# Optimization experiments

Measured on AMD Instinct MI355X. Metric: run time of the kernel, lower is better.

Reference implementation:

```python
import jax, jax.numpy as jnp
import numpy as np

B, NI, NA, D = 16, 2048, 2048, 256

def setup_inputs() -> dict:
    key = jax.random.key(0)
    k1, k2, k3 = jax.random.split(key, 3)
    input_seq = jax.random.normal(k1, (B, NI, D), dtype=jnp.float32)
    attendee_seq = jax.random.normal(k2, (B, NA, D), dtype=jnp.float32)
    # glorot-ish scale for bilinear weight
    W = jax.random.normal(k3, (D, D), dtype=jnp.float32) * (1.0 / np.sqrt(D))
    return {"input_seq": input_seq, "attendee_seq": attendee_seq, "W": W}

def reference(input_seq, attendee_seq, W):
    # bilinear scores: (x_i W) . a_j   -> [B, NI, NA]
    xW = jnp.einsum('bid,de->bie', input_seq, W)
    scores = jnp.einsum('bie,bje->bij', xW, attendee_seq)
    A = jax.nn.softmax(scores, axis=2)                 # softmax over attendee axis
    # weighted context: sum_j A[b,i,j] * v[b,j,:] -> [B, NI, D]
    attended = jnp.einsum('bij,bjd->bid', A, attendee_seq)
    return attended
```

## Files before the change

### kernel.cpp

```cpp
#include <hip/hip_runtime.h>
#include <hip/hip_bf16.h>

#define BB 16
#define NI 2048
#define NA 2048
#define DD 256
#define KVB 32
#define NT (NA / KVB)

typedef _Float16 half8 __attribute__((ext_vector_type(8)));
typedef __attribute__((ext_vector_type(16))) float f32x16;
typedef __attribute__((ext_vector_type(4))) float f32x4;
typedef __attribute__((ext_vector_type(4))) unsigned int uint4v;

typedef const unsigned int CGU __attribute__((address_space(1)));
typedef unsigned int LU __attribute__((address_space(3)));

static __device__ __forceinline__ unsigned short f2h(float f) {
  union { _Float16 h; unsigned short u; } x; x.h = (_Float16)f; return x.u;
}
static __device__ __forceinline__ float h2f(unsigned short u) {
  union { _Float16 h; unsigned short u; } x; x.u = u; return (float)x.h;
}
static __device__ __forceinline__ unsigned int pk2(float a, float b) {
  return __builtin_bit_cast(unsigned int, __builtin_amdgcn_cvt_pkrtz(a, b));
}
static __device__ __forceinline__ float ex2(float x) {
  return __builtin_amdgcn_exp2f(x);
}
static __device__ __forceinline__ void gload16(const unsigned short* g, unsigned short* l) {
  __builtin_amdgcn_global_load_lds((CGU*)g, (LU*)l, 16, 0, 0);
}

__global__ void prep_kernel(const float* __restrict__ a,
                            unsigned short* __restrict__ kfrag,
                            unsigned short* __restrict__ vfrag,
                            const float* __restrict__ w,
                            unsigned short* __restrict__ wbfh,
                            unsigned short* __restrict__ wbfl) {
  __shared__ float t[64][65];
  int bx = blockIdx.x;
  int tid = threadIdx.x;
  int rr = tid >> 4, c4 = tid & 15;

  if (bx >= 2048) {
    int r = bx - 2048;
    int dt = r >> 2, et4 = r & 3;
    int d0 = dt * 64, e0 = et4 * 64;
    int cc = c4 * 4;
#pragma unroll
    for (int k = 0; k < 4; ++k) {
      int row = rr + k * 16;
      float4 v = *(const float4*)(w + (size_t)(d0 + row) * DD + e0 + cc);
      t[row][cc + 0] = v.x; t[row][cc + 1] = v.y; t[row][cc + 2] = v.z; t[row][cc + 3] = v.w;
    }
    __syncthreads();
    int d = d0 + cc;
    int c = d >> 5;
    int quad = (d >> 3) & 3;
#pragma unroll
    for (int k = 0; k < 4; ++k) {
      int e_local = rr + k * 16;
      int eg = e0 + e_local;
      ushort4 h, l;
      float v0 = t[cc + 0][e_local]; h.x = f2h(v0); l.x = f2h(v0 - h2f(h.x));
      float v1 = t[cc + 1][e_local]; h.y = f2h(v1); l.y = f2h(v1 - h2f(h.y));
      float v2 = t[cc + 2][e_local]; h.z = f2h(v2); l.z = f2h(v2 - h2f(h.z));
      float v3 = t[cc + 3][e_local]; h.w = f2h(v3); l.w = f2h(v3 - h2f(h.w));
      int et = eg >> 4, l16e = eg & 15;
      size_t off = ((size_t)(et * 8 + c) * 64 + quad * 16 + l16e) * 8 + (c4 & 1) * 4;
      *(ushort4*)(wbfh + off) = h;
      *(ushort4*)(wbfl + off) = l;
    }
    return;
  }

  int b = bx >> 7;
  int r = bx & 127;
  int jt_t = r >> 2, dt_t = r & 3;
  int j0 = jt_t * 64, d0 = dt_t * 64;
#pragma unroll
  for (int k = 0; k < 4; ++k) {
    int row = rr + k * 16;
    int j = j0 + row;
    int d = d0 + c4 * 4;
    float4 v = *(const float4*)(a + ((size_t)b * NA + j) * DD + d);
    ushort4 hh;
    hh.x = f2h(v.x); hh.y = f2h(v.y); hh.z = f2h(v.z); hh.w = f2h(v.w);
    int kt = j >> 5;
    int ks = d >> 4;
    int lk = (j & 31) + 32 * ((d >> 3) & 1);
    *(ushort4*)(kfrag + (((size_t)b * NT + kt) * 16 + ks) * 512 + lk * 8 + (c4 & 1) * 4) = hh;
    t[row][c4 * 4 + 0] = v.x; t[row][c4 * 4 + 1] = v.y;
    t[row][c4 * 4 + 2] = v.z; t[row][c4 * 4 + 3] = v.w;
  }
  __syncthreads();
#pragma unroll
  for (int k = 0; k < 4; ++k) {
    int dl = rr + k * 16;
    int d = d0 + dl;
    int j = j0 + c4 * 4;
    ushort4 o;
    o.x = f2h(t[c4 * 4 + 0][dl]); o.y = f2h(t[c4 * 4 + 1][dl]);
    o.z = f2h(t[c4 * 4 + 2][dl]); o.w = f2h(t[c4 * 4 + 3][dl]);
    int kt = j >> 5;
    int hi = c4 & 1;
    int m = (c4 >> 2) & 1;
    int ebase = ((c4 >> 1) & 1) * 4;
    int hh_ = d >> 7, dtl = (d >> 5) & 3;
    int lv = (d & 31) + 32 * hi;
    *(ushort4*)(vfrag + ((((((size_t)b * NT + kt) * 2 + hh_) * 4 + dtl) * 2 + m) * 512) + lv * 8 + ebase) = o;
  }
}

__global__ __launch_bounds__(256, 8) void qgemm_kernel(
    const float* __restrict__ x, const unsigned short* __restrict__ wbfh,
    const unsigned short* __restrict__ wbfl, unsigned short* __restrict__ qfrag) {
  const int tid = threadIdx.x;
  const int lane = tid & 63;
  const int wv = tid >> 6;
  const int quad = lane >> 4;
  const int l16 = lane & 15;
  const int m0 = blockIdx.x * 64;

  half8 xf[8];
  {
    const float* xr = x + (size_t)(m0 + wv * 16 + l16) * DD;
#pragma unroll
    for (int c = 0; c < 8; ++c) {
      float4 a = *(const float4*)(xr + c * 32 + quad * 8);
      float4 b = *(const float4*)(xr + c * 32 + quad * 8 + 4);
      half8 v;
      v[0] = (_Float16)a.x; v[1] = (_Float16)a.y; v[2] = (_Float16)a.z; v[3] = (_Float16)a.w;
      v[4] = (_Float16)b.x; v[5] = (_Float16)b.y; v[6] = (_Float16)b.z; v[7] = (_Float16)b.w;
      xf[c] = v;
    }
  }

  const int sub = l16 & 7;
  const int khalf = (l16 >> 3) & 1;
#pragma unroll 1
  for (int et = 0; et < 16; ++et) {
    f32x4 acc; acc[0] = acc[1] = acc[2] = acc[3] = 0.f;
#pragma unroll
    for (int c = 0; c < 8; ++c) {
      half8 wh = *(const half8*)(wbfh + ((size_t)(et * 8 + c) * 64 + lane) * 8);
      half8 wl = *(const half8*)(wbfl + ((size_t)(et * 8 + c) * 64 + lane) * 8);
      acc = __builtin_amdgcn_mfma_f32_16x16x32_f16(xf[c], wh, acc, 0, 0, 0);
      acc = __builtin_amdgcn_mfma_f32_16x16x32_f16(xf[c], wl, acc, 0, 0, 0);
    }
#pragma unroll
    for (int rg = 0; rg < 4; ++rg) {
      int qrow = m0 + wv * 16 + 4 * quad + rg;
      int qt = qrow >> 5, l31q = qrow & 31;
      qfrag[((size_t)(qt * 16 + et)) * 512 + (l31q + 32 * khalf) * 8 + sub] =
          f2h(acc[rg] * 1.44269504f);
    }
  }
}

__global__ __launch_bounds__(256, 2) void attn_kernel(
    const unsigned short* __restrict__ kfrag, const unsigned short* __restrict__ vfrag,
    const unsigned short* __restrict__ qfrag, float* __restrict__ out) {
  __shared__ unsigned short kls[2][KVB * DD];

  const int tid = threadIdx.x;
  const int lane = tid & 63;
  const int wv = tid >> 6;
  const int pr = wv >> 1;
  const int h = wv & 1;
  const int l31 = lane & 31;
  const int hi = lane >> 5;

  int bx = blockIdx.x;
  int lbx = (bx & 7) * 64 + (bx >> 3);
  const int b = lbx >> 5;
  const int qbase = (lbx & 31) * 64 + pr * 32;

  const unsigned short* kfb = kfrag + (size_t)b * NT * 8192;

  half8 qh[16];
  {
    const unsigned short* qr = qfrag + ((size_t)((b * NI + qbase) >> 5) * 16) * 512 + lane * 8;
#pragma unroll
    for (int ks = 0; ks < 16; ++ks)
      qh[ks] = *(const half8*)(qr + ks * 512);
  }

  f32x16 acc[4];
#pragma unroll
  for (int dt = 0; dt < 4; ++dt)
#pragma unroll
    for (int i = 0; i < 16; ++i) acc[dt][i] = 0.f;
  float m0r = -INFINITY;
  float l0 = 0.f;

  const unsigned short* vp = vfrag + (((size_t)b * NT * 2 + h) * 4) * 1024 + lane * 8;
  const unsigned short* sp = kfb + 8192 + (wv * 512 + lane * 8);

#pragma unroll
  for (int i = 0; i < 4; ++i) {
    int off = (i * 4 + wv) * 512;
    gload16(kfb + off + lane * 8, &kls[0][off]);
  }
  __syncthreads();

#pragma unroll 1
  for (int kt = 0; kt < NT; ++kt) {
    half8 vb[8];
#pragma unroll
    for (int i = 0; i < 8; ++i)
      vb[i] = *(const half8*)(vp + i * 512);

    if (kt + 1 < NT) {
      unsigned short* d = &kls[(kt + 1) & 1][wv * 512];
      gload16(sp + 0 * 2048, d + 0 * 2048);
      gload16(sp + 1 * 2048, d + 1 * 2048);
      gload16(sp + 2 * 2048, d + 2 * 2048);
      gload16(sp + 3 * 2048, d + 3 * 2048);
    }

    const unsigned short* kb = &kls[kt & 1][0];
    f32x16 sA, sB;
#pragma unroll
    for (int i = 0; i < 16; ++i) { sA[i] = 0.f; sB[i] = 0.f; }
    __builtin_amdgcn_s_setprio(1);
#pragma unroll
    for (int ks = 0; ks < 8; ++ks) {
      half8 ka = *(const half8*)(kb + ks * 512 + lane * 8);
      sA = __builtin_amdgcn_mfma_f32_32x32x16_f16(ka, qh[ks], sA, 0, 0, 0);
    }
#pragma unroll
    for (int ks = 8; ks < 16; ++ks) {
      half8 ka = *(const half8*)(kb + ks * 512 + lane * 8);
      sB = __builtin_amdgcn_mfma_f32_32x32x16_f16(ka, qh[ks], sB, 0, 0, 0);
    }
    __builtin_amdgcn_s_setprio(0);
    float p[16];
#pragma unroll
    for (int i = 0; i < 16; ++i) p[i] = sA[i] + sB[i];

    float mt = p[0];
#pragma unroll
    for (int i = 1; i < 16; ++i) mt = fmaxf(mt, p[i]);
    mt = fmaxf(mt, __shfl_xor(mt, 32));
    if (__any(mt > m0r + 11.5416f)) {
      float mn = fmaxf(m0r, mt);
      float sc = ex2(m0r - mn);
      l0 *= sc;
#pragma unroll
      for (int dt = 0; dt < 4; ++dt)
#pragma unroll
        for (int i = 0; i < 16; ++i) acc[dt][i] *= sc;
      m0r = mn;
    }

#pragma unroll
    for (int i = 0; i < 16; ++i) p[i] = ex2(p[i] - m0r);
    l0 += (((p[0] + p[1]) + (p[2] + p[3])) + ((p[4] + p[5]) + (p[6] + p[7]))) +
          (((p[8] + p[9]) + (p[10] + p[11])) + ((p[12] + p[13]) + (p[14] + p[15])));

    half8 pa0, pa1;
    {
      uint4v u0 = { pk2(p[0], p[1]), pk2(p[2], p[3]), pk2(p[4], p[5]), pk2(p[6], p[7]) };
      uint4v u1 = { pk2(p[8], p[9]), pk2(p[10], p[11]), pk2(p[12], p[13]), pk2(p[14], p[15]) };
      pa0 = __builtin_bit_cast(half8, u0);
      pa1 = __builtin_bit_cast(half8, u1);
    }

    __builtin_amdgcn_s_setprio(1);
#pragma unroll
    for (int dt = 0; dt < 4; ++dt) {
      acc[dt] = __builtin_amdgcn_mfma_f32_32x32x16_f16(vb[dt * 2 + 0], pa0, acc[dt], 0, 0, 0);
      acc[dt] = __builtin_amdgcn_mfma_f32_32x32x16_f16(vb[dt * 2 + 1], pa1, acc[dt], 0, 0, 0);
    }
    __builtin_amdgcn_s_setprio(0);

    vp += 8192;
    sp += 8192;
    __syncthreads();
  }

  l0 += __shfl_xor(l0, 32);
  float inv0 = 1.0f / l0;
  float* ob = out + ((size_t)b * NI + qbase + l31) * DD + h * 128 + hi * 4;
#pragma unroll
  for (int dt = 0; dt < 4; ++dt) {
#pragma unroll
    for (int rq = 0; rq < 4; ++rq) {
      float4 v;
      v.x = acc[dt][rq * 4 + 0] * inv0;
      v.y = acc[dt][rq * 4 + 1] * inv0;
      v.z = acc[dt][rq * 4 + 2] * inv0;
      v.w = acc[dt][rq * 4 + 3] * inv0;
      *(float4*)(ob + dt * 32 + rq * 8) = v;
    }
  }
}

extern "C" void kernel_launch(void* const* d_in, const int* in_sizes, int n_in,
                              void* d_out, int out_size, void* d_ws, size_t ws_size,
                              hipStream_t stream) {
  const float* x = (const float*)d_in[0];
  const float* att = (const float*)d_in[1];
  const float* W = (const float*)d_in[2];
  float* out = (float*)d_out;

  const size_t NE = (size_t)BB * NA * DD;
  unsigned short* w0    = (unsigned short*)d_ws;
  unsigned short* kfrag = w0;
  unsigned short* vfrag = w0 + NE;
  unsigned short* qfrag = w0 + 2 * NE;
  unsigned short* wbfh  = w0 + 3 * NE;
  unsigned short* wbfl  = w0 + 3 * NE + 65536;

  prep_kernel<<<2064, 256, 0, stream>>>(att, kfrag, vfrag, W, wbfh, wbfl);
  qgemm_kernel<<<512, 256, 0, stream>>>(x, wbfh, wbfl, qfrag);
  attn_kernel<<<512, 256, 0, stream>>>(kfrag, vfrag, qfrag, out);
}
```

Measured before the change: 162.3 us.

## Load K fragments directly from global into registers, dropping LDS staging

Removes the double-buffered LDS staging of K tiles (global_load_lds plus per-iteration __syncthreads). Each wave now loads its K fragments straight from global memory into registers, and the two score MFMA chains are interleaved. This eliminates LDS traffic and block-wide barriers. In exchange, each of the four waves separately fetches the same K tile (relying on cache), raises register pressure, and loses the prefetch overlap of the next tile.

After: 178.5 us. 10.0% more time.

```diff
diff --git a/kernel.cpp b/kernel.cpp
--- a/kernel.cpp
+++ b/kernel.cpp
@@ -13,9 +13,6 @@
 typedef __attribute__((ext_vector_type(4))) float f32x4;
 typedef __attribute__((ext_vector_type(4))) unsigned int uint4v;
 
-typedef const unsigned int CGU __attribute__((address_space(1)));
-typedef unsigned int LU __attribute__((address_space(3)));
-
 static __device__ __forceinline__ unsigned short f2h(float f) {
   union { _Float16 h; unsigned short u; } x; x.h = (_Float16)f; return x.u;
 }
@@ -27,9 +24,6 @@
 }
 static __device__ __forceinline__ float ex2(float x) {
   return __builtin_amdgcn_exp2f(x);
-}
-static __device__ __forceinline__ void gload16(const unsigned short* g, unsigned short* l) {
-  __builtin_amdgcn_global_load_lds((CGU*)g, (LU*)l, 16, 0, 0);
 }
 
 __global__ void prep_kernel(const float* __restrict__ a,
@@ -162,8 +156,6 @@
 __global__ __launch_bounds__(256, 2) void attn_kernel(
     const unsigned short* __restrict__ kfrag, const unsigned short* __restrict__ vfrag,
     const unsigned short* __restrict__ qfrag, float* __restrict__ out) {
-  __shared__ unsigned short kls[2][KVB * DD];
-
   const int tid = threadIdx.x;
   const int lane = tid & 63;
   const int wv = tid >> 6;
@@ -177,8 +169,6 @@
   const int b = lbx >> 5;
   const int qbase = (lbx & 31) * 64 + pr * 32;
 
-  const unsigned short* kfb = kfrag + (size_t)b * NT * 8192;
-
   half8 qh[16];
   {
     const unsigned short* qr = qfrag + ((size_t)((b * NI + qbase) >> 5) * 16) * 512 + lane * 8;
@@ -195,45 +185,32 @@
   float m0r = -INFINITY;
   float l0 = 0.f;
 
+  const unsigned short* kp = kfrag + (size_t)b * NT * 8192 + lane * 8;
   const unsigned short* vp = vfrag + (((size_t)b * NT * 2 + h) * 4) * 1024 + lane * 8;
-  const unsigned short* sp = kfb + 8192 + (wv * 512 + lane * 8);
-
-#pragma unroll
-  for (int i = 0; i < 4; ++i) {
-    int off = (i * 4 + wv) * 512;
-    gload16(kfb + off + lane * 8, &kls[0][off]);
-  }
-  __syncthreads();
 
 #pragma unroll 1
   for (int kt = 0; kt < NT; ++kt) {
+    half8 ka[8], kb2[8];
+#pragma unroll
+    for (int ks = 0; ks < 8; ++ks)
+      ka[ks] = *(const half8*)(kp + ks * 512);
+#pragma unroll
+    for (int ks = 0; ks < 8; ++ks)
+      kb2[ks] = *(const half8*)(kp + (8 + ks) * 512);
+
     half8 vb[8];
 #pragma unroll
     for (int i = 0; i < 8; ++i)
       vb[i] = *(const half8*)(vp + i * 512);
 
-    if (kt + 1 < NT) {
-      unsigned short* d = &kls[(kt + 1) & 1][wv * 512];
-      gload16(sp + 0 * 2048, d + 0 * 2048);
-      gload16(sp + 1 * 2048, d + 1 * 2048);
-      gload16(sp + 2 * 2048, d + 2 * 2048);
-      gload16(sp + 3 * 2048, d + 3 * 2048);
-    }
-
-    const unsigned short* kb = &kls[kt & 1][0];
     f32x16 sA, sB;
 #pragma unroll
     for (int i = 0; i < 16; ++i) { sA[i] = 0.f; sB[i] = 0.f; }
     __builtin_amdgcn_s_setprio(1);
 #pragma unroll
     for (int ks = 0; ks < 8; ++ks) {
-      half8 ka = *(const half8*)(kb + ks * 512 + lane * 8);
-      sA = __builtin_amdgcn_mfma_f32_32x32x16_f16(ka, qh[ks], sA, 0, 0, 0);
-    }
-#pragma unroll
-    for (int ks = 8; ks < 16; ++ks) {
-      half8 ka = *(const half8*)(kb + ks * 512 + lane * 8);
-      sB = __builtin_amdgcn_mfma_f32_32x32x16_f16(ka, qh[ks], sB, 0, 0, 0);
+      sA = __builtin_amdgcn_mfma_f32_32x32x16_f16(ka[ks], qh[ks], sA, 0, 0, 0);
+      sB = __builtin_amdgcn_mfma_f32_32x32x16_f16(kb2[ks], qh[8 + ks], sB, 0, 0, 0);
     }
     __builtin_amdgcn_s_setprio(0);
     float p[16];
@@ -276,9 +253,8 @@
     }
     __builtin_amdgcn_s_setprio(0);
 
+    kp += 8192;
     vp += 8192;
-    sp += 8192;
-    __syncthreads();
   }
 
   l0 += __shfl_xor(l0, 32);
```

## Split attention over two KV halves and merge partials in a combine kernel

Applied to the files above, without the earlier changes.

The attention kernel now splits the key/value sequence into two halves, launching twice as many blocks, each covering half the KV tiles. Each block writes a normalized fp16 partial output plus its running max and sum, and a new combine kernel rescales and merges the two partials into the fp32 output. Launch bounds are raised to three blocks per SM. The aim is better occupancy and load balance across the 256 CUs, since 512 blocks at two per CU left many CUs idle. The cost is an extra kernel launch, extra global traffic for the partials, and fp16 rounding of the intermediate outputs.

New measurement: 356.4 us. 120% more time.

```diff
diff --git a/kernel.cpp b/kernel.cpp
--- a/kernel.cpp
+++ b/kernel.cpp
@@ -7,6 +7,8 @@
 #define DD 256
 #define KVB 32
 #define NT (NA / KVB)
+#define NTL (NT / 2)
+#define QTOT (BB * NI)
 
 typedef _Float16 half8 __attribute__((ext_vector_type(8)));
 typedef __attribute__((ext_vector_type(16))) float f32x16;
@@ -159,9 +161,10 @@
   }
 }
 
-__global__ __launch_bounds__(256, 2) void attn_kernel(
+__global__ __launch_bounds__(256, 3) void attn_kernel(
     const unsigned short* __restrict__ kfrag, const unsigned short* __restrict__ vfrag,
-    const unsigned short* __restrict__ qfrag, float* __restrict__ out) {
+    const unsigned short* __restrict__ qfrag, unsigned short* __restrict__ op,
+    float* __restrict__ mlf) {
   __shared__ unsigned short kls[2][KVB * DD];
 
   const int tid = threadIdx.x;
@@ -173,11 +176,13 @@
   const int hi = lane >> 5;
 
   int bx = blockIdx.x;
-  int lbx = (bx & 7) * 64 + (bx >> 3);
-  const int b = lbx >> 5;
-  const int qbase = (lbx & 31) * 64 + pr * 32;
-
-  const unsigned short* kfb = kfrag + (size_t)b * NT * 8192;
+  int lbx = (bx & 7) * 128 + (bx >> 3);
+  const int sk = lbx >> 9;
+  const int rem = lbx & 511;
+  const int b = rem >> 5;
+  const int qbase = (rem & 31) * 64 + pr * 32;
+
+  const unsigned short* kfb = kfrag + ((size_t)b * NT + sk * NTL) * 8192;
 
   half8 qh[16];
   {
@@ -195,7 +200,7 @@
   float m0r = -INFINITY;
   float l0 = 0.f;
 
-  const unsigned short* vp = vfrag + (((size_t)b * NT * 2 + h) * 4) * 1024 + lane * 8;
+  const unsigned short* vp = vfrag + (((size_t)(b * NT + sk * NTL) * 2 + h) * 4) * 1024 + lane * 8;
   const unsigned short* sp = kfb + 8192 + (wv * 512 + lane * 8);
 
 #pragma unroll
@@ -206,13 +211,13 @@
   __syncthreads();
 
 #pragma unroll 1
-  for (int kt = 0; kt < NT; ++kt) {
+  for (int kt = 0; kt < NTL; ++kt) {
     half8 vb[8];
 #pragma unroll
     for (int i = 0; i < 8; ++i)
       vb[i] = *(const half8*)(vp + i * 512);
 
-    if (kt + 1 < NT) {
+    if (kt + 1 < NTL) {
       unsigned short* d = &kls[(kt + 1) & 1][wv * 512];
       gload16(sp + 0 * 2048, d + 0 * 2048);
       gload16(sp + 1 * 2048, d + 1 * 2048);
@@ -283,19 +288,52 @@
 
   l0 += __shfl_xor(l0, 32);
   float inv0 = 1.0f / l0;
-  float* ob = out + ((size_t)b * NI + qbase + l31) * DD + h * 128 + hi * 4;
+  unsigned short* opb = op + ((size_t)sk * QTOT + (size_t)b * NI + qbase + l31) * DD + h * 128 + hi * 4;
 #pragma unroll
   for (int dt = 0; dt < 4; ++dt) {
 #pragma unroll
     for (int rq = 0; rq < 4; ++rq) {
-      float4 v;
-      v.x = acc[dt][rq * 4 + 0] * inv0;
-      v.y = acc[dt][rq * 4 + 1] * inv0;
-      v.z = acc[dt][rq * 4 + 2] * inv0;
-      v.w = acc[dt][rq * 4 + 3] * inv0;
-      *(float4*)(ob + dt * 32 + rq * 8) = v;
-    }
-  }
+      ushort4 v;
+      v.x = f2h(acc[dt][rq * 4 + 0] * inv0);
+      v.y = f2h(acc[dt][rq * 4 + 1] * inv0);
+      v.z = f2h(acc[dt][rq * 4 + 2] * inv0);
+      v.w = f2h(acc[dt][rq * 4 + 3] * inv0);
+      *(ushort4*)(opb + dt * 32 + rq * 8) = v;
+    }
+  }
+  if (h == 0 && hi == 0) {
+    float2* mlp = (float2*)mlf;
+    mlp[(size_t)sk * QTOT + (size_t)b * NI + qbase + l31] = make_float2(m0r, l0);
+  }
+}
+
+__global__ __launch_bounds__(256) void combine_kernel(
+    const unsigned short* __restrict__ op, const float* __restrict__ mlf,
+    float* __restrict__ out) {
+  size_t t = (size_t)blockIdx.x * 256 + threadIdx.x;
+  size_t base = t * 8;
+  size_t q = base >> 8;
+  const float2* mlp = (const float2*)mlf;
+  float2 ml0 = mlp[q];
+  float2 ml1 = mlp[(size_t)QTOT + q];
+  float M = fmaxf(ml0.x, ml1.x);
+  float w0 = ml0.y * ex2(ml0.x - M);
+  float w1 = ml1.y * ex2(ml1.x - M);
+  float inv = 1.0f / (w0 + w1);
+  float a0 = w0 * inv, a1 = w1 * inv;
+  half8 p0 = *(const half8*)(op + base);
+  half8 p1 = *(const half8*)(op + (size_t)QTOT * DD + base);
+  float4 r0, r1;
+  r0.x = a0 * (float)p0[0] + a1 * (float)p1[0];
+  r0.y = a0 * (float)p0[1] + a1 * (float)p1[1];
+  r0.z = a0 * (float)p0[2] + a1 * (float)p1[2];
+  r0.w = a0 * (float)p0[3] + a1 * (float)p1[3];
+  r1.x = a0 * (float)p0[4] + a1 * (float)p1[4];
+  r1.y = a0 * (float)p0[5] + a1 * (float)p1[5];
+  r1.z = a0 * (float)p0[6] + a1 * (float)p1[6];
+  r1.w = a0 * (float)p0[7] + a1 * (float)p1[7];
+  *(float4*)(out + base) = r0;
+  *(float4*)(out + base + 4) = r1;
 }
 
 extern "C" void kernel_launch(void* const* d_in, const int* in_sizes, int n_in,
@@ -313,8 +351,11 @@
   unsigned short* qfrag = w0 + 2 * NE;
   unsigned short* wbfh  = w0 + 3 * NE;
   unsigned short* wbfl  = w0 + 3 * NE + 65536;
+  unsigned short* op    = w0 + 3 * NE + 131072;
+  float* mlf            = (float*)(w0 + 5 * NE + 131072);
 
   prep_kernel<<<2064, 256, 0, stream>>>(att, kfrag, vfrag, W, wbfh, wbfl);
   qgemm_kernel<<<512, 256, 0, stream>>>(x, wbfh, wbfl, qfrag);
-  attn_kernel<<<512, 256, 0, stream>>>(kfrag, vfrag, qfrag, out);
-}
+  attn_kernel<<<1024, 256, 0, stream>>>(kfrag, vfrag, qfrag, op, mlf);
+  combine_kernel<<<4096, 256, 0, stream>>>(op, mlf, out);
+}
```
